# Performance work log

Measured on AMD Instinct MI355X. Metric: run time of the kernel, lower is better.

The kernel has to match this reference:

```python
import jax, jax.numpy as jnp
import numpy as np
from jax import lax

B, C_IN = 8192, 1

def _conv(x, w, b):
    # x: [N,C,H,W], w: [O,I,kh,kw] valid conv, stride 1
    y = lax.conv_general_dilated(x, w, window_strides=(1, 1), padding='VALID',
                                 dimension_numbers=('NCHW', 'OIHW', 'NCHW'))
    return y + b[None, :, None, None]

def _maxpool2(x):
    return lax.reduce_window(x, -jnp.inf, lax.max, (1, 1, 2, 2), (1, 1, 2, 2), 'VALID')

def setup_inputs() -> dict:
    key = jax.random.key(0)
    ks = jax.random.split(key, 9)
    def kaiming(k, shape, fan_in):
        return jax.random.normal(k, shape, jnp.float32) * np.float32(1.0 / np.sqrt(fan_in))
    x = jax.random.normal(ks[0], (B, C_IN, 28, 28), jnp.float32)
    w1 = kaiming(ks[1], (10, C_IN, 5, 5), C_IN * 25)
    b1 = kaiming(ks[2], (10,), C_IN * 25)
    w2 = kaiming(ks[3], (20, 10, 5, 5), 10 * 25)
    b2 = kaiming(ks[4], (20,), 10 * 25)
    wl1 = kaiming(ks[5], (50, 320), 320)
    bl1 = kaiming(ks[6], (50,), 320)
    wl2 = kaiming(ks[7], (10, 50), 50)
    bl2 = kaiming(ks[8], (10,), 50)
    return {"x": x, "w1": w1, "b1": b1, "w2": w2, "b2": b2,
            "wl1": wl1, "bl1": bl1, "wl2": wl2, "bl2": bl2}

def reference(x, w1, b1, w2, b2, wl1, bl1, wl2, bl2):
    h = jax.nn.relu(_conv(x, w1, b1))       # [B,10,24,24]
    h = _maxpool2(h)                         # [B,10,12,12]
    h = jax.nn.relu(_conv(h, w2, b2))        # [B,20,8,8]
    h = _maxpool2(h)                         # [B,20,4,4]
    h = h.reshape(h.shape[0], -1)            # [B,320]
    h = jax.nn.relu(h @ wl1.T + bl1)         # [B,50]
    return h @ wl2.T + bl2                   # [B,10]
```

## Files before the change

kernel.cpp:

```cpp
#include <hip/hip_runtime.h>

#define THREADS 256
#define IPB 4

typedef _Float16 f16;
typedef _Float16 f16x2 __attribute__((ext_vector_type(2)));
typedef _Float16 f16x8 __attribute__((ext_vector_type(8)));
typedef float f32x4 __attribute__((ext_vector_type(4)));
typedef float f32x16 __attribute__((ext_vector_type(16)));
typedef unsigned int uint;

__device__ __forceinline__ f16x2 pkrtz(float a, float b) {
    return __builtin_bit_cast(f16x2, __builtin_amdgcn_cvt_pkrtz(a, b));
}
template<int CTRL>
__device__ __forceinline__ float dppmax(float v) {
    const int i = __builtin_bit_cast(int, v);
    const int s = __builtin_amdgcn_update_dpp(i, i, CTRL, 0xF, 0xF, true);
    return fmaxf(v, __builtin_bit_cast(float, s));
}

#define P1_ROW 400
#define P1_IMG 4784

__global__ void pack_weights(const float* __restrict__ w1,
                             const float* __restrict__ w2,
                             const float* __restrict__ wl1,
                             unsigned char* __restrict__ ws) {
    uint* w1pk  = (uint*)ws;
    f16x8* w2af = (f16x8*)(ws + 1024);
    f16x8* wl1pk = (f16x8*)(ws + 17408);
    const int gid = blockIdx.x * blockDim.x + threadIdx.x;
    const int gsz = gridDim.x * blockDim.x;
    for (int i = gid; i < 250; i += gsz) {
        const unsigned short u =
            __builtin_bit_cast(unsigned short, (f16)w1[i]);
        w1pk[i] = (uint)u | ((uint)u << 16);
    }
    for (int e = gid; e < 1000; e += gsz) {
        const int s = e / 40, r = e - s * 40;
        const int oc = r >> 1, h = r & 1;
        f16x8 a;
        #pragma unroll
        for (int j = 0; j < 8; ++j) {
            const int ic = h * 8 + j;
            a[j] = (f16)(ic < 10 ? w2[(oc * 10 + ic) * 25 + s] : 0.f);
        }
        w2af[e] = a;
    }
    for (int e = gid; e < 2560; e += gsz) {
        const int tile = e / 640, rem = e % 640;
        const int s = rem / 64, lane = rem % 64;
        const int m = lane & 15, quad = lane >> 4;
        const int hh = tile * 16 + m;
        f16x8 a;
        #pragma unroll
        for (int j = 0; j < 8; ++j)
            a[j] = (f16)(hh < 50 ? wl1[hh * 320 + s * 32 + quad * 8 + j] : 0.f);
        wl1pk[e] = a;
    }
}

__global__ __launch_bounds__(THREADS, 7)
void lenet_one(const float* __restrict__ x,
               const unsigned char* __restrict__ ws, const float* __restrict__ b1,
               const float* __restrict__ b2,
               const float* __restrict__ bl1,
               const float* __restrict__ wl2, const float* __restrict__ bl2,
               float* __restrict__ out, int batch)
{
    __shared__ __align__(16) unsigned char p1c[IPB * P1_IMG];
    __shared__ __align__(16) f16 p2h[IPB * 320];
    __shared__ float h1[IPB * 52];

    const uint*  w1pk  = (const uint*)ws;
    const f16x8* w2af  = (const f16x8*)(ws + 1024);
    const f16x8* wl1pk = (const f16x8*)(ws + 17408);

    const int tid = threadIdx.x;
    const int lane = tid & 63;
    const int wv_ = tid >> 6;
    const int cM = lane & 31, hK = lane >> 5;

    {
        const int img = wv_;
        const int imgg = min(blockIdx.x * IPB + img, batch - 1);
        const float* xim = x + (size_t)imgg * 784;
        for (int pq = lane; pq < 144; pq += 64) {
            const int py = pq / 12, px = pq % 12;
            const float* xb = xim + (2 * py) * 28 + 2 * px;
            float win[36];
            #pragma unroll
            for (int r = 0; r < 6; ++r)
                #pragma unroll
                for (int cc = 0; cc < 6; ++cc)
                    win[r * 6 + cc] = xb[r * 28 + cc];
            f16x2 pr[30];
            #pragma unroll
            for (int r = 0; r < 6; ++r)
                #pragma unroll
                for (int cc = 0; cc < 5; ++cc)
                    pr[r * 5 + cc] = pkrtz(win[r * 6 + cc], win[r * 6 + cc + 1]);
            f16 ch[10];
            #pragma unroll
            for (int c = 0; c < 10; ++c) {
                f16x2 accT = {(f16)0.f, (f16)0.f};
                f16x2 accB = {(f16)0.f, (f16)0.f};
                #pragma unroll
                for (int ky = 0; ky < 5; ++ky)
                    #pragma unroll
                    for (int kx = 0; kx < 5; ++kx) {
                        const uint wp = w1pk[c * 25 + ky * 5 + kx];
                        const f16x2 wv = __builtin_bit_cast(f16x2, wp);
                        accT += pr[ky * 5 + kx] * wv;
                        accB += pr[(ky + 1) * 5 + kx] * wv;
                    }
                const float q0 = fmaxf((float)accT[0], (float)accB[0]);
                const float q1 = fmaxf((float)accT[1], (float)accB[1]);
                ch[c] = (f16)fmaxf(fmaxf(q0, q1) + b1[c], 0.f);
            }
            f16x8 v0, v1;
            #pragma unroll
            for (int j = 0; j < 8; ++j) v0[j] = ch[j];
            v1[0] = ch[8]; v1[1] = ch[9];
            #pragma unroll
            for (int j = 2; j < 8; ++j) v1[j] = (f16)0.f;
            unsigned char* dst = p1c + img * P1_IMG + py * P1_ROW + px * 32;
            *(f16x8*)(dst)      = v0;
            *(f16x8*)(dst + 16) = v1;
        }
    }
    __syncthreads();

    {
        const int cy = cM >> 3, cx = cM & 7;
        const int afoff = (cM < 20 ? cM : 19) * 2 + hK;
        int bb[2];
        #pragma unroll
        for (int q = 0; q < 2; ++q) {
            const int t = wv_ * 2 + q, im = t >> 1, h2 = t & 1;
            bb[q] = im * P1_IMG + (4 * h2 + cy) * P1_ROW + cx * 32 + hK * 16;
        }
        f32x16 acc[2];
        #pragma unroll
        for (int q = 0; q < 2; ++q)
            #pragma unroll
            for (int r = 0; r < 16; ++r) acc[q][r] = 0.f;
        #pragma unroll 1
        for (int ky = 0; ky < 5; ++ky) {
            #pragma unroll
            for (int kx = 0; kx < 5; ++kx) {
                const f16x8 a = w2af[(ky * 5 + kx) * 40 + afoff];
                #pragma unroll
                for (int q = 0; q < 2; ++q) {
                    const f16x8 b =
                        *(const f16x8*)(p1c + bb[q] + ky * P1_ROW + kx * 32);
                    acc[q] = __builtin_amdgcn_mfma_f32_32x32x16_f16(a, b, acc[q],
                                                                    0, 0, 0);
                }
            }
        }
        #pragma unroll
        for (int q = 0; q < 2; ++q) {
            const int t = wv_ * 2 + q, im = t >> 1, h2 = t & 1;
            #pragma unroll
            for (int r = 0; r < 16; ++r) {
                const int m = (r & 3) + 8 * (r >> 2) + 4 * hK;
                float v = acc[q][r];
                v = dppmax<0xB1>(v);
                v = dppmax<0x128>(v);
                if (m < 20 && (lane & 9) == 0) {
                    const int py = 2 * h2 + (cM >> 4), px = cx >> 1;
                    p2h[im * 320 + m * 16 + py * 4 + px] =
                        (f16)fmaxf(v + b2[m], 0.f);
                }
            }
        }
    }
    __syncthreads();

    {
        const int n = lane & 15, quad = lane >> 4;
        f32x4 facc = {0.f, 0.f, 0.f, 0.f};
        #pragma unroll 1
        for (int s = 0; s < 10; ++s) {
            const f16x8 a = wl1pk[(wv_ * 10 + s) * 64 + lane];
            f16x8 b = {};
            if (n < IPB)
                b = *(const f16x8*)(p2h + n * 320 + s * 32 + quad * 8);
            facc = __builtin_amdgcn_mfma_f32_16x16x32_f16(a, b, facc, 0, 0, 0);
        }
        if (n < IPB) {
            #pragma unroll
            for (int r = 0; r < 4; ++r) {
                const int h = wv_ * 16 + quad * 4 + r;
                if (h < 50)
                    h1[n * 52 + h] = fmaxf(facc[r] + bl1[h], 0.f);
            }
        }
    }
    __syncthreads();

    if (tid < IPB * 10) {
        const int im = tid / 10, o = tid % 10;
        const int imgo = min(blockIdx.x * IPB + im, batch - 1);
        float a = bl2[o];
        #pragma unroll
        for (int h = 0; h < 50; ++h)
            a += h1[im * 52 + h] * wl2[o * 50 + h];
        out[(size_t)imgo * 10 + o] = a;
    }
}

extern "C" void kernel_launch(void* const* d_in, const int* in_sizes, int n_in,
                              void* d_out, int out_size, void* d_ws, size_t ws_size,
                              hipStream_t stream) {
    const float* x   = (const float*)d_in[0];
    const float* w1  = (const float*)d_in[1];
    const float* b1  = (const float*)d_in[2];
    const float* w2  = (const float*)d_in[3];
    const float* b2  = (const float*)d_in[4];
    const float* wl1 = (const float*)d_in[5];
    const float* bl1 = (const float*)d_in[6];
    const float* wl2 = (const float*)d_in[7];
    const float* bl2 = (const float*)d_in[8];
    float* out = (float*)d_out;
    unsigned char* ws = (unsigned char*)d_ws;

    const int batch = in_sizes[0] / 784;
    pack_weights<<<16, 256, 0, stream>>>(w1, w2, wl1, ws);
    const int grid = (batch + IPB - 1) / IPB;
    lenet_one<<<grid, THREADS, 0, stream>>>(x, ws, b1, b2, bl1, wl2, bl2,
                                            out, batch);
}
```

Before: 140.8 us.

## Give each wave a private image pipeline and replace block barriers with wave fences

Each wave now owns one image's LDS region (conv1 output, pooled conv2 output, FC1 activations) and runs the whole network for that image. The three __syncthreads calls become an s_waitcnt lgkmcnt(0) fence, so waves in a block no longer wait on each other and can drift apart to overlap memory and MFMA work. In exchange, the FC1 MFMA stage now issues four tiles per wave with only one useful batch column, which multiplies FC1 matrix work per block. The final FC2 stage also runs on 10 lanes per wave.

Result: no change. 143.0 us (+1.5%).

```diff
diff --git a/kernel.cpp b/kernel.cpp
--- a/kernel.cpp
+++ b/kernel.cpp
@@ -19,9 +19,12 @@
     const int s = __builtin_amdgcn_update_dpp(i, i, CTRL, 0xF, 0xF, true);
     return fmaxf(v, __builtin_bit_cast(float, s));
 }
+__device__ __forceinline__ void wave_fence() {
+    asm volatile("s_waitcnt lgkmcnt(0)" ::: "memory");
+}
 
 #define P1_ROW 400
-#define P1_IMG 4784
+#define WAVE_LDS 5632
 
 __global__ void pack_weights(const float* __restrict__ w1,
                              const float* __restrict__ w2,
@@ -69,9 +72,7 @@
                const float* __restrict__ wl2, const float* __restrict__ bl2,
                float* __restrict__ out, int batch)
 {
-    __shared__ __align__(16) unsigned char p1c[IPB * P1_IMG];
-    __shared__ __align__(16) f16 p2h[IPB * 320];
-    __shared__ float h1[IPB * 52];
+    __shared__ __align__(16) unsigned char lds[IPB * WAVE_LDS];
 
     const uint*  w1pk  = (const uint*)ws;
     const f16x8* w2af  = (const f16x8*)(ws + 1024);
@@ -82,10 +83,14 @@
     const int wv_ = tid >> 6;
     const int cM = lane & 31, hK = lane >> 5;
 
-    {
-        const int img = wv_;
-        const int imgg = min(blockIdx.x * IPB + img, batch - 1);
-        const float* xim = x + (size_t)imgg * 784;
+    unsigned char* wbase = lds + wv_ * WAVE_LDS;
+    f16*   p2h = (f16*)(wbase + 4784);
+    float* h1  = (float*)(wbase + 5424);
+
+    const int img = min(blockIdx.x * IPB + wv_, batch - 1);
+
+    {
+        const float* xim = x + (size_t)img * 784;
         for (int pq = lane; pq < 144; pq += 64) {
             const int py = pq / 12, px = pq % 12;
             const float* xb = xim + (2 * py) * 28 + 2 * px;
@@ -125,23 +130,21 @@
             v1[0] = ch[8]; v1[1] = ch[9];
             #pragma unroll
             for (int j = 2; j < 8; ++j) v1[j] = (f16)0.f;
-            unsigned char* dst = p1c + img * P1_IMG + py * P1_ROW + px * 32;
+            unsigned char* dst = wbase + py * P1_ROW + px * 32;
             *(f16x8*)(dst)      = v0;
             *(f16x8*)(dst + 16) = v1;
         }
     }
-    __syncthreads();
-
+    wave_fence();
+
+    f32x16 acc[2];
     {
         const int cy = cM >> 3, cx = cM & 7;
         const int afoff = (cM < 20 ? cM : 19) * 2 + hK;
         int bb[2];
         #pragma unroll
-        for (int q = 0; q < 2; ++q) {
-            const int t = wv_ * 2 + q, im = t >> 1, h2 = t & 1;
-            bb[q] = im * P1_IMG + (4 * h2 + cy) * P1_ROW + cx * 32 + hK * 16;
-        }
-        f32x16 acc[2];
+        for (int q = 0; q < 2; ++q)
+            bb[q] = (4 * q + cy) * P1_ROW + cx * 32 + hK * 16;
         #pragma unroll
         for (int q = 0; q < 2; ++q)
             #pragma unroll
@@ -154,15 +157,18 @@
                 #pragma unroll
                 for (int q = 0; q < 2; ++q) {
                     const f16x8 b =
-                        *(const f16x8*)(p1c + bb[q] + ky * P1_ROW + kx * 32);
+                        *(const f16x8*)(wbase + bb[q] + ky * P1_ROW + kx * 32);
                     acc[q] = __builtin_amdgcn_mfma_f32_32x32x16_f16(a, b, acc[q],
                                                                     0, 0, 0);
                 }
             }
         }
+    }
+
+    {
+        const int cx = cM & 7;
         #pragma unroll
         for (int q = 0; q < 2; ++q) {
-            const int t = wv_ * 2 + q, im = t >> 1, h2 = t & 1;
             #pragma unroll
             for (int r = 0; r < 16; ++r) {
                 const int m = (r & 3) + 8 * (r >> 2) + 4 * hK;
@@ -170,45 +176,51 @@
                 v = dppmax<0xB1>(v);
                 v = dppmax<0x128>(v);
                 if (m < 20 && (lane & 9) == 0) {
-                    const int py = 2 * h2 + (cM >> 4), px = cx >> 1;
-                    p2h[im * 320 + m * 16 + py * 4 + px] =
-                        (f16)fmaxf(v + b2[m], 0.f);
+                    const int py = 2 * q + (cM >> 4), px = cx >> 1;
+                    p2h[m * 16 + py * 4 + px] = (f16)fmaxf(v + b2[m], 0.f);
                 }
             }
         }
     }
-    __syncthreads();
+    wave_fence();
 
     {
         const int n = lane & 15, quad = lane >> 4;
-        f32x4 facc = {0.f, 0.f, 0.f, 0.f};
+        f32x4 facc[4] = {{0.f,0.f,0.f,0.f},{0.f,0.f,0.f,0.f},
+                         {0.f,0.f,0.f,0.f},{0.f,0.f,0.f,0.f}};
         #pragma unroll 1
         for (int s = 0; s < 10; ++s) {
-            const f16x8 a = wl1pk[(wv_ * 10 + s) * 64 + lane];
             f16x8 b = {};
-            if (n < IPB)
-                b = *(const f16x8*)(p2h + n * 320 + s * 32 + quad * 8);
-            facc = __builtin_amdgcn_mfma_f32_16x16x32_f16(a, b, facc, 0, 0, 0);
-        }
-        if (n < IPB) {
-            #pragma unroll
-            for (int r = 0; r < 4; ++r) {
-                const int h = wv_ * 16 + quad * 4 + r;
-                if (h < 50)
-                    h1[n * 52 + h] = fmaxf(facc[r] + bl1[h], 0.f);
-            }
-        }
-    }
-    __syncthreads();
-
-    if (tid < IPB * 10) {
-        const int im = tid / 10, o = tid % 10;
-        const int imgo = min(blockIdx.x * IPB + im, batch - 1);
+            if (n == 0)
+                b = *(const f16x8*)((const unsigned char*)p2h +
+                                    s * 64 + quad * 16);
+            #pragma unroll
+            for (int ht = 0; ht < 4; ++ht) {
+                const f16x8 a = wl1pk[(ht * 10 + s) * 64 + lane];
+                facc[ht] = __builtin_amdgcn_mfma_f32_16x16x32_f16(a, b, facc[ht],
+                                                                  0, 0, 0);
+            }
+        }
+        if (n == 0) {
+            #pragma unroll
+            for (int ht = 0; ht < 4; ++ht)
+                #pragma unroll
+                for (int r = 0; r < 4; ++r) {
+                    const int h = ht * 16 + quad * 4 + r;
+                    if (h < 50)
+                        h1[h] = fmaxf(facc[ht][r] + bl1[h], 0.f);
+                }
+        }
+    }
+    wave_fence();
+
+    if (lane < 10) {
+        const int o = lane;
         float a = bl2[o];
         #pragma unroll
         for (int h = 0; h < 50; ++h)
-            a += h1[im * 52 + h] * wl2[o * 50 + h];
-        out[(size_t)imgo * 10 + o] = a;
+            a += h1[h] * wl2[o * 50 + h];
+        out[(size_t)img * 10 + o] = a;
     }
 }
 
```
